# Optimization experiments

Measured on AMD Instinct MI355X. Metric: run time of the kernel, lower is better.

## Reference

```python
import jax, jax.numpy as jnp
import numpy as np

N = 50000          # nodes per node type
F = 256            # input feature dim
C = 256            # hidden_channels
H, D = 8, 32       # heads, head_dim (C = H*D)
E = 200000         # edges per edge type
OUT = 16           # out_channels
SRC = (0, 1, 0)    # edge type -> source node-type index (user,item)
DST = (1, 0, 0)    # edge type -> destination node-type index
LABELED = 1        # labeled_class = 'item'


def setup_inputs() -> dict:
    key = jax.random.key(0)
    ks = jax.random.split(key, 24)
    s = 0.06  # ~1/sqrt(256) init scale
    inp = {
        'x': jax.random.normal(ks[0], (2, N, F), jnp.float32),
        'edge_index': jax.random.randint(ks[1], (3, 2, E), 0, N, jnp.int64),
        'lin_w': jax.random.normal(ks[2], (2, F, C), jnp.float32) * s,
        'lin_b': jnp.zeros((2, C), jnp.float32),
        'k_w': jax.random.normal(ks[3], (2, C, C), jnp.float32) * s,
        'k_b': jnp.zeros((2, C), jnp.float32),
        'q_w': jax.random.normal(ks[4], (2, C, C), jnp.float32) * s,
        'q_b': jnp.zeros((2, C), jnp.float32),
        'v_w': jax.random.normal(ks[5], (2, C, C), jnp.float32) * s,
        'v_b': jnp.zeros((2, C), jnp.float32),
        'a_w': jax.random.normal(ks[6], (2, C, C), jnp.float32) * s,
        'a_b': jnp.zeros((2, C), jnp.float32),
        'skip': jnp.ones((2,), jnp.float32),
        'a_rel': jax.random.normal(ks[7], (3, H, D, D), jnp.float32) * (1.0 / np.sqrt(D)),
        'm_rel': jax.random.normal(ks[8], (3, H, D, D), jnp.float32) * (1.0 / np.sqrt(D)),
        'p_rel': jnp.ones((3, H), jnp.float32),
        'out_w': jax.random.normal(ks[9], (C, OUT), jnp.float32) * s,
        'out_b': jnp.zeros((OUT,), jnp.float32),
    }
    return inp


def _segment_softmax(alpha, idx, n):
    # alpha: [E, H], idx: [E] destination node ids
    amax = jax.ops.segment_max(alpha, idx, num_segments=n)
    amax = jnp.where(jnp.isfinite(amax), amax, 0.0)
    ex = jnp.exp(alpha - amax[idx])
    den = jax.ops.segment_sum(ex, idx, num_segments=n)
    return ex / (den[idx] + 1e-16)


def reference(x, edge_index, lin_w, lin_b, k_w, k_b, q_w, q_b, v_w, v_b,
              a_w, a_b, skip, a_rel, m_rel, p_rel, out_w, out_b):
    # per-node-type input Linear + ReLU
    h = jax.nn.relu(jnp.einsum('tnf,tfc->tnc', x, lin_w) + lin_b[:, None, :])

    def proj(w, b):
        return (jnp.einsum('tnc,tce->tne', h, w) + b[:, None, :]).reshape(2, N, H, D)

    k = proj(k_w, k_b)
    q = proj(q_w, q_b)
    v = proj(v_w, v_b)

    agg = jnp.zeros((2, N, H, D), h.dtype)
    for t in range(3):  # fixed small loop over edge types
        s, d = SRC[t], DST[t]
        src_idx, dst_idx = edge_index[t, 0], edge_index[t, 1]
        # relation-specific transforms of source keys / values
        k_rel = jnp.einsum('nhd,hde->nhe', k[s], a_rel[t])
        v_rel = jnp.einsum('nhd,hde->nhe', v[s], m_rel[t])
        # per-edge attention logits [E, H]
        alpha = (q[d][dst_idx] * k_rel[src_idx]).sum(-1) * p_rel[t] / (D ** 0.5)
        alpha = _segment_softmax(alpha, dst_idx, N)
        msg = v_rel[src_idx] * alpha[..., None]          # [E, H, D]
        agg = agg.at[d].add(jax.ops.segment_sum(msg, dst_idx, num_segments=N))

    o = agg.reshape(2, N, C)
    o = jnp.einsum('tnc,tce->tne', jax.nn.gelu(o, approximate=False), a_w) + a_b[:, None, :]
    beta = jax.nn.sigmoid(skip)[:, None, None]
    o = beta * o + (1.0 - beta) * h                      # skip connection (in == out dims)

    return o[LABELED] @ out_w + out_b                    # logits for labeled_class='item'
```

## Files before the change

### kernel.cpp

```cpp
#include <hip/hip_runtime.h>
#include <hip/hip_bf16.h>

using u16 = unsigned short;
using u32 = unsigned int;

#define NNODES 50000
#define NEDGE  200000
#define DEGCAP 64
#define NT     3125

__device__ __forceinline__ float blo2f(u32 u) { u32 v = u << 16; float f; __builtin_memcpy(&f, &v, 4); return f; }
__device__ __forceinline__ float bhi2f(u32 u) { u32 v = u & 0xffff0000u; float f; __builtin_memcpy(&f, &v, 4); return f; }
__device__ __forceinline__ u16 f2b(float f) {
  __hip_bfloat16 h = __float2bfloat16(f);
  u16 r; __builtin_memcpy(&r, &h, 2); return r;
}
__device__ __forceinline__ float gelu_exact(float x) {
  return 0.5f * x * (1.f + erff(x * 0.70710678118654752f));
}

__device__ __forceinline__ void gload16(const void* gp, void* lp) {
  __builtin_amdgcn_global_load_lds(
      (__attribute__((address_space(1))) u32*)(const_cast<void*>(gp)),
      (__attribute__((address_space(3))) u32*)lp, 16, 0, 0);
}
__device__ __forceinline__ void gload16_nt(const void* gp, void* lp) {
  __builtin_amdgcn_global_load_lds(
      (__attribute__((address_space(1))) u32*)(const_cast<void*>(gp)),
      (__attribute__((address_space(3))) u32*)lp, 16, 0, 2);
}

#define WAIT_VM(N) asm volatile("s_waitcnt vmcnt(" #N ")" ::: "memory")

typedef __bf16 bh8 __attribute__((ext_vector_type(8)));
typedef float f32x4 __attribute__((ext_vector_type(4)));

struct GArg { const u16* A; const u16* B; const float* bias; u16* C; };

__device__ __forceinline__ void stage_blk_bf16(const u16* At, u16* buf, int wave, int lane) {
#pragma unroll
  for (int i = 0; i < 2; ++i) {
    const int row = wave * 4 + i * 2 + (lane >> 5);
    const int c   = (lane & 31) ^ (row & 7);
    gload16(At + (size_t)row * 256 + c * 8, buf + wave * 1024 + i * 512 + lane * 8);
  }
}

__device__ __forceinline__ void stage_blk_f32(const float* At, float* buf, int wave, int lane) {
#pragma unroll
  for (int i = 0; i < 4; ++i) {
    const int row = wave * 4 + i;
    const int c   = lane ^ (row & 7);
    gload16_nt(At + (size_t)row * 256 + c * 4, buf + row * 256 + lane * 4);
  }
}

template <int MODE, bool F32A>
__launch_bounds__(256, 2)
__global__ void gemm_v10(GArg g0, GArg g1, GArg g2)
{
  GArg ga = (blockIdx.z == 0) ? g0 : ((blockIdx.z == 1) ? g1 : g2);
  const int tid  = threadIdx.x;
  const int lane = tid & 63;
  const int wave = tid >> 6;
  const int lr = lane & 15;
  const int lq = lane >> 4;
  const int colbase = wave * 64;

  constexpr int TW = F32A ? 8192 : 4096;
  __shared__ alignas(16) u16 lds[3][TW];
  __shared__ alignas(16) u16 pat[4][1152];
  u16* wl = &pat[wave][0];

  bh8 B[4][8];
#pragma unroll
  for (int s = 0; s < 4; ++s) {
    const u16* bp = ga.B + (size_t)(colbase + s * 16 + lr) * 256 + lq * 8;
#pragma unroll
    for (int ks = 0; ks < 8; ++ks) B[s][ks] = *(const bh8*)(bp + ks * 32);
  }
  float bias[4];
#pragma unroll
  for (int s = 0; s < 4; ++s) bias[s] = ga.bias[colbase + s * 16 + lr];

  int foffL[8], foffH[8];
#pragma unroll
  for (int ks = 0; ks < 8; ++ks) {
    if (F32A) {
      foffL[ks] = lr * 256 + (((ks * 8 + lq * 2)     ^ (lr & 7)) << 2);
      foffH[ks] = lr * 256 + (((ks * 8 + lq * 2 + 1) ^ (lr & 7)) << 2);
    } else {
      foffL[ks] = lr * 256 + (((ks * 4 + lq) ^ (lr & 7)) * 8);
    }
  }

  const int t0 = blockIdx.x;
  const int ts = gridDim.x;

  if (F32A) stage_blk_f32((const float*)ga.A + (size_t)t0 * 4096, (float*)&lds[0][0], wave, lane);
  else      stage_blk_bf16(ga.A + (size_t)t0 * 4096, &lds[0][0], wave, lane);
  if (t0 + ts < NT) {
    if (F32A) stage_blk_f32((const float*)ga.A + (size_t)(t0 + ts) * 4096, (float*)&lds[1][0], wave, lane);
    else      stage_blk_bf16(ga.A + (size_t)(t0 + ts) * 4096, &lds[1][0], wave, lane);
  }

  int it = 0, rb = 0;
  for (int t = t0; t < NT; t += ts, ++it) {
    const bool p1 = (t + ts < NT), p2 = (t + 2 * ts < NT);
    if (p2) {
      const int rn = (rb + 2 >= 3) ? rb - 1 : rb + 2;
      if (F32A) stage_blk_f32((const float*)ga.A + (size_t)(t + 2 * ts) * 4096, (float*)&lds[rn][0], wave, lane);
      else      stage_blk_bf16(ga.A + (size_t)(t + 2 * ts) * 4096, &lds[rn][0], wave, lane);
    }
    if (!p1)            { WAIT_VM(0); }
    else if (!p2)       { if (F32A) { WAIT_VM(6); }  else { WAIT_VM(4); } }
    else if (it >= 2)   { if (F32A) { WAIT_VM(12); } else { WAIT_VM(8); } }
    else                { if (F32A) { WAIT_VM(8); }  else { WAIT_VM(4); } }
    __builtin_amdgcn_s_barrier();

    bh8 ab[8];
    if (F32A) {
      const float* fbuf = (const float*)&lds[rb][0];
#pragma unroll
      for (int ks = 0; ks < 8; ++ks) {
        const f32x4 lo = *(const f32x4*)(fbuf + foffL[ks]);
        const f32x4 hi = *(const f32x4*)(fbuf + foffH[ks]);
#pragma unroll
        for (int j = 0; j < 4; ++j) { ab[ks][j] = (__bf16)lo[j]; ab[ks][j + 4] = (__bf16)hi[j]; }
      }
    } else {
      const u16* buf = &lds[rb][0];
#pragma unroll
      for (int ks = 0; ks < 8; ++ks) ab[ks] = *(const bh8*)(buf + foffL[ks]);
    }

    f32x4 acc[4];
#pragma unroll
    for (int s = 0; s < 4; ++s) acc[s] = (f32x4){0.f, 0.f, 0.f, 0.f};
#pragma unroll
    for (int ks = 0; ks < 8; ++ks) {
#pragma unroll
      for (int s = 0; s < 4; ++s)
        acc[s] = __builtin_amdgcn_mfma_f32_16x16x32_bf16(ab[ks], B[s][ks], acc[s], 0, 0, 0);
    }

#pragma unroll
    for (int s = 0; s < 4; ++s) {
#pragma unroll
      for (int r = 0; r < 4; ++r) {
        float v = acc[s][r] + bias[s];
        if (MODE == 0) v = fmaxf(v, 0.f);
        wl[(lq * 4 + r) * 72 + s * 16 + lr] = f2b(v);
      }
    }
#pragma unroll
    for (int j = 0; j < 2; ++j) {
      const int row = (lane >> 3) + j * 8;
      const int seg = lane & 7;
      const uint4 pv = *(const uint4*)(wl + row * 72 + seg * 8);
      *(uint4*)(ga.C + ((size_t)t * 16 + row) * 256 + colbase + seg * 8) = pv;
    }
    __builtin_amdgcn_s_barrier();
    rb = (rb + 1 == 3) ? 0 : rb + 1;
  }
}

__global__ void prep_w_k(const float* __restrict__ lin_w, const float* __restrict__ q_w,
                         const float* __restrict__ a_w, const float* __restrict__ k_w,
                         const float* __restrict__ v_w, const float* __restrict__ k_b,
                         const float* __restrict__ v_b, const float* __restrict__ a_rel,
                         const float* __restrict__ m_rel, const float* __restrict__ out_w,
                         const float* __restrict__ a_b, const float* __restrict__ out_b,
                         const float* __restrict__ skipv,
                         u16* __restrict__ lin0T, u16* __restrict__ lin1T,
                         u16* __restrict__ qT,
                         u16* __restrict__ kfT, u16* __restrict__ vfT,
                         u16* __restrict__ WcT, float* __restrict__ bfin,
                         float* __restrict__ bkf, float* __restrict__ bvf,
                         int* __restrict__ cnt)
{
  const int tid = blockIdx.x * 256 + threadIdx.x;
  const int nn = tid >> 8, kk = tid & 255;
  switch (blockIdx.y) {
    case 0: lin0T[tid] = f2b(lin_w[kk * 256 + nn]); break;
    case 1: lin1T[tid] = f2b(lin_w[65536 + kk * 256 + nn]); break;
    case 2: qT[tid] = f2b(q_w[65536 + kk * 256 + nn]); break;
    case 3: {
      const int h = nn >> 5, e = nn & 31;
      float s = 0.f;
      for (int d = 0; d < 32; ++d) s += k_w[kk * 256 + h * 32 + d] * a_rel[(h * 32 + d) * 32 + e];
      kfT[tid] = f2b(s);
      if (kk == 0) {
        float sb = 0.f;
        for (int d = 0; d < 32; ++d) sb += k_b[h * 32 + d] * a_rel[(h * 32 + d) * 32 + e];
        bkf[nn] = sb;
      }
      break;
    }
    case 4: {
      const int h = nn >> 5, e = nn & 31;
      float s = 0.f;
      for (int d = 0; d < 32; ++d) s += v_w[kk * 256 + h * 32 + d] * m_rel[(h * 32 + d) * 32 + e];
      vfT[tid] = f2b(s);
      if (kk == 0) {
        float sb = 0.f;
        for (int d = 0; d < 32; ++d) sb += v_b[h * 32 + d] * m_rel[(h * 32 + d) * 32 + e];
        bvf[nn] = sb;
      }
      break;
    }
    case 5: {
      const float beta = 1.f / (1.f + __expf(-skipv[1]));
      if (tid < 8192) {
        const int j = tid & 15;
        const int k = tid >> 4;
        float s;
        if (k < 256) {
          float acc = 0.f;
          for (int d = 0; d < 256; ++d)
            acc += a_w[65536 + k * 256 + d] * out_w[d * 16 + j];
          s = beta * acc;
        } else {
          s = (1.f - beta) * out_w[(k - 256) * 16 + j];
        }
        WcT[j * 512 + k] = f2b(s);
      }
      if (tid < 16) {
        float acc = 0.f;
        for (int c = 0; c < 256; ++c) acc += a_b[256 + c] * out_w[c * 16 + tid];
        bfin[tid] = beta * acc + out_b[tid];
      }
      break;
    }
    default:
      if (tid < NNODES) cnt[tid] = 0;
      break;
  }
}

__global__ void scatter_k(const int* __restrict__ ei, int* __restrict__ cnt, int* __restrict__ srcl) {
  const int e = blockIdx.x * 256 + threadIdx.x;
  if (e >= NEDGE) return;
  const int src = ei[e];
  const int dst = ei[NEDGE + e];
  if ((unsigned)dst >= NNODES || (unsigned)src >= NNODES) return;
  const int pos = atomicAdd(&cnt[dst], 1);
  if (pos < DEGCAP) srcl[(size_t)dst * DEGCAP + pos] = src;
}

__global__ void edge_agg_k(const u16* __restrict__ qb, const u16* __restrict__ krel,
                           const u16* __restrict__ vrel, const int* __restrict__ cnt,
                           const int* __restrict__ srcl, const float* __restrict__ prel,
                           u16* __restrict__ g)
{
  const int node = (blockIdx.x * blockDim.x + threadIdx.x) >> 6;
  if (node >= NNODES) return;
  const int lane = threadIdx.x & 63;
  const int hh = lane >> 3;
  const int off = hh * 32 + (lane & 7) * 4;
  const float scale = prel[hh] * 0.17677669529663687f;
  const uint2 qv = *(const uint2*)(qb + (size_t)node * 256 + off);
  const float q0 = blo2f(qv.x) * scale, q1 = bhi2f(qv.x) * scale;
  const float q2 = blo2f(qv.y) * scale, q3 = bhi2f(qv.y) * scale;
  int dg = cnt[node]; if (dg > DEGCAP) dg = DEGCAP;
  const int mysrc = srcl[(size_t)node * DEGCAP + lane];

  float den = 0.f, a0 = 0.f, a1 = 0.f, a2 = 0.f, a3 = 0.f;
  uint2 kv = {0, 0}, vv = {0, 0};
  if (dg > 0) {
    const int s0 = __shfl(mysrc, 0);
    kv = *(const uint2*)(krel + (size_t)s0 * 256 + off);
    vv = *(const uint2*)(vrel + (size_t)s0 * 256 + off);
  }
  for (int i = 0; i < dg; ++i) {
    uint2 kn = kv, vn = vv;
    if (i + 1 < dg) {
      const int sn = __shfl(mysrc, i + 1);
      kn = *(const uint2*)(krel + (size_t)sn * 256 + off);
      vn = *(const uint2*)(vrel + (size_t)sn * 256 + off);
    }
    float p = q0 * blo2f(kv.x) + q1 * bhi2f(kv.x) + q2 * blo2f(kv.y) + q3 * bhi2f(kv.y);
    p += __shfl_xor(p, 1);
    p += __shfl_xor(p, 2);
    p += __shfl_xor(p, 4);
    const float ex = __expf(p);
    den += ex;
    a0 += ex * blo2f(vv.x); a1 += ex * bhi2f(vv.x);
    a2 += ex * blo2f(vv.y); a3 += ex * bhi2f(vv.y);
    kv = kn; vv = vn;
  }
  float r0 = 0.f, r1 = 0.f, r2 = 0.f, r3 = 0.f;
  if (dg > 0) {
    const float inv = 1.f / den;
    r0 = gelu_exact(a0 * inv); r1 = gelu_exact(a1 * inv);
    r2 = gelu_exact(a2 * inv); r3 = gelu_exact(a3 * inv);
  }
  uint2 gv;
  gv.x = (u32)f2b(r0) | ((u32)f2b(r1) << 16);
  gv.y = (u32)f2b(r2) | ((u32)f2b(r3) << 16);
  *(uint2*)(g + (size_t)node * 256 + off) = gv;
}

__launch_bounds__(256, 3)
__global__ void final_v10(const u16* __restrict__ g, const u16* __restrict__ h1,
                          const u16* __restrict__ WcT, const float* __restrict__ bfin,
                          float* __restrict__ out)
{
  const int tid = threadIdx.x;
  const int lane = tid & 63;
  const int wave = tid >> 6;
  const int lr = lane & 15;
  const int lq = lane >> 4;

  __shared__ alignas(16) u16 lds[3][8192];
  __shared__ float red[4][256];

  bh8 B[4];
  {
    const u16* bp = WcT + (size_t)lr * 512 + wave * 128 + lq * 8;
#pragma unroll
    for (int ks = 0; ks < 4; ++ks) B[ks] = *(const bh8*)(bp + ks * 32);
  }
  const float bv = bfin[tid & 15];

  int foff[4];
#pragma unroll
  for (int ks = 0; ks < 4; ++ks)
    foff[ks] = wave * 2048 + lr * 128 + (((ks * 4 + lq) ^ (lr & 7)) * 8);

  const u16* srcq = (wave < 2) ? g + wave * 128 : h1 + (wave - 2) * 128;

  const int t0 = blockIdx.x;
  const int ts = gridDim.x;

#define FSTAGE(T, RB)                                                          \
  {                                                                            \
    _Pragma("unroll")                                                          \
    for (int i = 0; i < 4; ++i) {                                              \
      const int row = i * 4 + (lane >> 4);                                     \
      const int c   = (lane & 15) ^ (row & 7);                                 \
      gload16(srcq + (size_t)(T) * 4096 + row * 256 + c * 8,                   \
              &lds[RB][wave * 2048 + i * 512 + lane * 8]);                     \
    }                                                                          \
  }

  FSTAGE(t0, 0);
  if (t0 + ts < NT) FSTAGE(t0 + ts, 1);

  int it = 0, rb = 0;
  for (int t = t0; t < NT; t += ts, ++it) {
    const bool p1 = (t + ts < NT), p2 = (t + 2 * ts < NT);
    if (p2) {
      const int rn = (rb + 2 >= 3) ? rb - 1 : rb + 2;
      FSTAGE(t + 2 * ts, rn);
    }
    if (!p1)          { WAIT_VM(0); }
    else if (!p2)     { WAIT_VM(4); }
    else if (it >= 2) { WAIT_VM(10); }
    else              { WAIT_VM(8); }
    __builtin_amdgcn_s_barrier();

    f32x4 acc = {0.f, 0.f, 0.f, 0.f};
    const u16* buf = &lds[rb][0];
#pragma unroll
    for (int ks = 0; ks < 4; ++ks)
      acc = __builtin_amdgcn_mfma_f32_16x16x32_bf16(*(const bh8*)(buf + foff[ks]), B[ks], acc, 0, 0, 0);

#pragma unroll
    for (int r = 0; r < 4; ++r) red[wave][(lq * 4 + r) * 16 + lr] = acc[r];
    asm volatile("s_waitcnt lgkmcnt(0)" ::: "memory");
    __builtin_amdgcn_s_barrier();

    const float s = red[0][tid] + red[1][tid] + red[2][tid] + red[3][tid] + bv;
    out[(size_t)t * 256 + tid] = s;
    __builtin_amdgcn_s_barrier();
    rb = (rb + 1 == 3) ? 0 : rb + 1;
  }
#undef FSTAGE
}

extern "C" void kernel_launch(void* const* d_in, const int* in_sizes, int n_in,
                              void* d_out, int out_size, void* d_ws, size_t ws_size,
                              hipStream_t stream)
{
  const float* x     = (const float*)d_in[0];
  const int*   ei    = (const int*)d_in[1];
  const float* lin_w = (const float*)d_in[2];
  const float* lin_b = (const float*)d_in[3];
  const float* k_w   = (const float*)d_in[4];
  const float* k_b   = (const float*)d_in[5];
  const float* q_w   = (const float*)d_in[6];
  const float* q_b   = (const float*)d_in[7];
  const float* v_w   = (const float*)d_in[8];
  const float* v_b   = (const float*)d_in[9];
  const float* a_w   = (const float*)d_in[10];
  const float* a_b   = (const float*)d_in[11];
  const float* skipv = (const float*)d_in[12];
  const float* a_rel = (const float*)d_in[13];
  const float* m_rel = (const float*)d_in[14];
  const float* p_rel = (const float*)d_in[15];
  const float* out_w = (const float*)d_in[16];
  const float* out_b = (const float*)d_in[17];
  char* ws = (char*)d_ws;

  u16*  h0    = (u16*)(ws + 0);
  u16*  h1    = (u16*)(ws + 25600000);
  u16*  qb    = (u16*)(ws + 51200000);
  u16*  krel  = (u16*)(ws + 76800000);
  u16*  vrel  = (u16*)(ws + 102400000);
  u16*  gbuf  = (u16*)(ws + 128000000);
  char* W     = ws + 153600000;
  u16*  lin0T = (u16*)(W + 0);
  u16*  lin1T = (u16*)(W + 131072);
  u16*  qT    = (u16*)(W + 2 * 131072);
  u16*  kfT   = (u16*)(W + 3 * 131072);
  u16*  vfT   = (u16*)(W + 4 * 131072);
  u16*  WcT   = (u16*)(W + 5 * 131072);
  float* bfin = (float*)(W + 5 * 131072 + 16384);
  float* bkf  = (float*)(W + 5 * 131072 + 17408);
  float* bvf  = (float*)(W + 5 * 131072 + 18432);
  int*  cnt   = (int*)(W + 5 * 131072 + 19456);
  int*  srcl  = (int*)(W + 5 * 131072 + 19456 + 200000);

  prep_w_k<<<dim3(256, 7), 256, 0, stream>>>(lin_w, q_w, a_w, k_w, v_w, k_b, v_b,
                                             a_rel, m_rel, out_w, a_b, out_b, skipv,
                                             lin0T, lin1T, qT, kfT, vfT, WcT, bfin,
                                             bkf, bvf, cnt);
  scatter_k<<<(NEDGE + 255) / 256, 256, 0, stream>>>(ei, cnt, srcl);

  {
    GArg a0{(const u16*)x, lin0T, lin_b, h0};
    GArg a1{(const u16*)(x + (size_t)NNODES * 256), lin1T, lin_b + 256, h1};
    gemm_v10<0, true><<<dim3(256, 1, 2), 256, 0, stream>>>(a0, a1, a0);
  }
  {
    GArg a0{h1, qT, q_b + 256, qb};
    GArg a1{h0, kfT, bkf, krel};
    GArg a2{h0, vfT, bvf, vrel};
    gemm_v10<1, false><<<dim3(170, 1, 3), 256, 0, stream>>>(a0, a1, a2);
  }
  edge_agg_k<<<12500, 256, 0, stream>>>(qb, krel, vrel, cnt, srcl, p_rel, gbuf);
  final_v10<<<768, 256, 0, stream>>>(gbuf, h1, WcT, bfin, (float*)d_out);
}
```

Measured before the change: 308.7 us.

## Fuse K and V projections into one kernel sharing staged h0 tiles

Adds a 512-thread kernel where four waves compute the K projection and four compute the V projection from the same 16-row h0 tile staged once in LDS, so h0 is read once for both instead of twice. The Q projection now runs alone in the existing GEMM with a larger grid. This trades an extra kernel launch and a heavier per-block register load of weights for less global traffic on h0.

```diff
diff --git a/kernel.cpp b/kernel.cpp
--- a/kernel.cpp
+++ b/kernel.cpp
@@ -44,6 +44,12 @@
     const int c   = (lane & 31) ^ (row & 7);
     gload16(At + (size_t)row * 256 + c * 8, buf + wave * 1024 + i * 512 + lane * 8);
   }
+}
+
+__device__ __forceinline__ void stage_blk8_bf16(const u16* At, u16* buf, int wave, int lane) {
+  const int row = wave * 2 + (lane >> 5);
+  const int c   = (lane & 31) ^ (row & 7);
+  gload16(At + (size_t)row * 256 + c * 8, buf + wave * 512 + lane * 8);
 }
 
 __device__ __forceinline__ void stage_blk_f32(const float* At, float* buf, int wave, int lane) {
@@ -159,6 +165,98 @@
       const int seg = lane & 7;
       const uint4 pv = *(const uint4*)(wl + row * 72 + seg * 8);
       *(uint4*)(ga.C + ((size_t)t * 16 + row) * 256 + colbase + seg * 8) = pv;
+    }
+    __builtin_amdgcn_s_barrier();
+    rb = (rb + 1 == 3) ? 0 : rb + 1;
+  }
+}
+
+__launch_bounds__(512, 2)
+__global__ void qkv8_k(const u16* __restrict__ h0,
+                       const u16* __restrict__ kfT, const u16* __restrict__ vfT,
+                       const float* __restrict__ bkf, const float* __restrict__ bvf,
+                       u16* __restrict__ krel, u16* __restrict__ vrel)
+{
+  const int tid  = threadIdx.x;
+  const int lane = tid & 63;
+  const int wave = tid >> 6;
+  const int lr = lane & 15;
+  const int lq = lane >> 4;
+  const int colbase = (wave & 3) * 64;
+  const bool isv = wave >= 4;
+
+  __shared__ alignas(16) u16 lds[3][4096];
+  __shared__ alignas(16) u16 pat[8][1152];
+  u16* wl = &pat[wave][0];
+
+  const u16* Bsrc = isv ? vfT : kfT;
+  u16* C = isv ? vrel : krel;
+  const float* bias_p = isv ? bvf : bkf;
+
+  bh8 B[4][8];
+#pragma unroll
+  for (int s = 0; s < 4; ++s) {
+    const u16* bp = Bsrc + (size_t)(colbase + s * 16 + lr) * 256 + lq * 8;
+#pragma unroll
+    for (int ks = 0; ks < 8; ++ks) B[s][ks] = *(const bh8*)(bp + ks * 32);
+  }
+  float bias[4];
+#pragma unroll
+  for (int s = 0; s < 4; ++s) bias[s] = bias_p[colbase + s * 16 + lr];
+
+  int foff[8];
+#pragma unroll
+  for (int ks = 0; ks < 8; ++ks)
+    foff[ks] = lr * 256 + (((ks * 4 + lq) ^ (lr & 7)) * 8);
+
+  const int t0 = blockIdx.x;
+  const int ts = gridDim.x;
+
+  stage_blk8_bf16(h0 + (size_t)t0 * 4096, &lds[0][0], wave, lane);
+  if (t0 + ts < NT) stage_blk8_bf16(h0 + (size_t)(t0 + ts) * 4096, &lds[1][0], wave, lane);
+
+  int it = 0, rb = 0;
+  for (int t = t0; t < NT; t += ts, ++it) {
+    const bool p1 = (t + ts < NT), p2 = (t + 2 * ts < NT);
+    if (p2) {
+      const int rn = (rb + 2 >= 3) ? rb - 1 : rb + 2;
+      stage_blk8_bf16(h0 + (size_t)(t + 2 * ts) * 4096, &lds[rn][0], wave, lane);
+    }
+    if (!p1)            { WAIT_VM(0); }
+    else if (!p2)       { WAIT_VM(4); }
+    else if (it >= 2)   { WAIT_VM(6); }
+    else if (it == 1)   { WAIT_VM(4); }
+    else                { WAIT_VM(2); }
+    __builtin_amdgcn_s_barrier();
+
+    const u16* buf = &lds[rb][0];
+    bh8 ab[8];
+#pragma unroll
+    for (int ks = 0; ks < 8; ++ks) ab[ks] = *(const bh8*)(buf + foff[ks]);
+
+    f32x4 acc[4];
+#pragma unroll
+    for (int s = 0; s < 4; ++s) acc[s] = (f32x4){0.f, 0.f, 0.f, 0.f};
+#pragma unroll
+    for (int ks = 0; ks < 8; ++ks) {
+#pragma unroll
+      for (int s = 0; s < 4; ++s)
+        acc[s] = __builtin_amdgcn_mfma_f32_16x16x32_bf16(ab[ks], B[s][ks], acc[s], 0, 0, 0);
+    }
+
+#pragma unroll
+    for (int s = 0; s < 4; ++s) {
+#pragma unroll
+      for (int r = 0; r < 4; ++r) {
+        wl[(lq * 4 + r) * 72 + s * 16 + lr] = f2b(acc[s][r] + bias[s]);
+      }
+    }
+#pragma unroll
+    for (int j = 0; j < 2; ++j) {
+      const int row = (lane >> 3) + j * 8;
+      const int seg = lane & 7;
+      const uint4 pv = *(const uint4*)(wl + row * 72 + seg * 8);
+      *(uint4*)(C + ((size_t)t * 16 + row) * 256 + colbase + seg * 8) = pv;
     }
     __builtin_amdgcn_s_barrier();
     rb = (rb + 1 == 3) ? 0 : rb + 1;
@@ -435,10 +533,10 @@
   }
   {
     GArg a0{h1, qT, q_b + 256, qb};
-    GArg a1{h0, kfT, bkf, krel};
-    GArg a2{h0, vfT, bvf, vrel};
-    gemm_v10<1, false><<<dim3(170, 1, 3), 256, 0, stream>>>(a0, a1, a2);
-  }
+    gemm_v10<1, false><<<dim3(512, 1, 1), 256, 0, stream>>>(a0, a0, a0);
+  }
+  qkv8_k<<<256, 512, 0, stream>>>(h0, kfT, vfT, bkf, bvf, krel, vrel);
+
   edge_agg_k<<<12500, 256, 0, stream>>>(qb, krel, vrel, cnt, srcl, p_rel, gbuf);
   final_v10<<<768, 256, 0, stream>>>(gbuf, h1, WcT, bfin, (float*)d_out);
 }
```

After: 321.8 us. 1.04x slower.
